# Performance work log

Measured on AMD Instinct MI355X. Metric: run time of the kernel, lower is better.

The kernel has to match this reference:

```python
import jax, jax.numpy as jnp
import numpy as np

BLANK = 0
NEG = jnp.float32(-1e30)  # finite stand-in for -inf (keeps logaddexp grads NaN-free)


def _ctc_loss(preds, targets, blank=BLANK):
    """CTC loss with fused log_softmax, zero_infinity, reduction='mean'.

    preds:   (N, T, C) raw logits
    targets: (N, L) int labels, 0 = padding/blank; target_lengths = count_nonzero
    """
    N, T, C = preds.shape
    L = targets.shape[1]
    S = 2 * L + 1  # extended label length (blanks interleaved)

    lp = jax.nn.log_softmax(preds, axis=-1)  # (N, T, C)

    # extended label sequence: blank, y1, blank, y2, ..., yL, blank
    ext = jnp.full((N, S), blank, dtype=targets.dtype).at[:, 1::2].set(targets)

    # gather log-probs of extended labels: (N, T, S) -> scan over T as (T, N, S)
    lp_ext = jax.vmap(lambda l, e: l[:, e])(lp, ext).transpose(1, 0, 2)

    # skip transition s-2 -> s allowed iff ext[s] != blank and ext[s] != ext[s-2]
    prev2 = jnp.pad(ext, ((0, 0), (2, 0)), constant_values=blank)[:, :S]
    skip_ok = (ext != blank) & (ext != prev2)  # (N, S)

    # alpha init at t=0
    alpha0 = jnp.full((N, S), NEG, dtype=lp.dtype)
    alpha0 = alpha0.at[:, 0].set(lp_ext[0, :, 0]).at[:, 1].set(lp_ext[0, :, 1])

    neg_col = jnp.full((N, 1), NEG, dtype=lp.dtype)

    def step(alpha, lp_t):
        a1 = jnp.concatenate([neg_col, alpha[:, :-1]], axis=1)
        a2 = jnp.concatenate([neg_col, neg_col, alpha[:, :-2]], axis=1)
        a2 = jnp.where(skip_ok, a2, NEG)
        alpha = jnp.logaddexp(jnp.logaddexp(alpha, a1), a2) + lp_t
        return alpha, None

    alpha, _ = jax.lax.scan(step, alpha0, lp_ext[1:])  # (N, S) at t = T-1

    tl = jnp.sum(targets != 0, axis=1)  # target lengths (pred lengths are all T)
    rows = jnp.arange(N)
    final = jnp.logaddexp(alpha[rows, 2 * tl], alpha[rows, 2 * tl - 1])

    # zero_infinity=True: zero out non-finite (vanished) losses
    loss = jnp.where(final < -1e29, 0.0, -final)
    # reduction='mean': divide each by its target length, then batch-mean
    return jnp.mean(loss / jnp.maximum(tl, 1).astype(loss.dtype))


def setup_inputs() -> dict:
    key = jax.random.key(0)
    k1, k2 = jax.random.split(key)
    preds = jax.random.normal(k1, (128, 1024, 256), dtype=jnp.float32)
    # labels in [1, C): nonzero so count_nonzero gives full target lengths
    targets = jax.random.randint(k2, (128, 128), 1, 256, dtype=jnp.int32)
    return {"preds": preds, "targets": targets}


def reference(preds, targets):
    return _ctc_loss(preds, targets)
```

## Files before the change

### kernel.cpp

```cpp
#include <hip/hip_runtime.h>

#define L2E 1.4426950408889634f
#define LN2D 0.6931471805599453

__device__ __forceinline__ void async_copy16(const float* g, float* l) {
    __builtin_amdgcn_global_load_lds(
        (const __attribute__((address_space(1))) void*)g,
        (__attribute__((address_space(3))) void*)l, 16, 0, 0);
}
__device__ __forceinline__ void wait_vm28() { __builtin_amdgcn_s_waitcnt(0x4F7C); }
__device__ __forceinline__ void wait_vm0()  { __builtin_amdgcn_s_waitcnt(0x0F70); }

__device__ __forceinline__ double dpp_sr1_f64(double x) {
    const int lo = __builtin_amdgcn_update_dpp(0, __double2loint(x), 0x138, 0xF, 0xF, true);
    const int hi = __builtin_amdgcn_update_dpp(0, __double2hiint(x), 0x138, 0xF, 0xF, true);
    return __hiloint2double(hi, lo);
}
__device__ __forceinline__ double dpp_sl1_f64(double x) {
    const int lo = __builtin_amdgcn_update_dpp(0, __double2loint(x), 0x130, 0xF, 0xF, true);
    const int hi = __builtin_amdgcn_update_dpp(0, __double2hiint(x), 0x130, 0xF, 0xF, true);
    return __hiloint2double(hi, lo);
}
__device__ __forceinline__ int wave_imax(int v) {
    int t;
#define DM(ctrl) t = __builtin_amdgcn_update_dpp(v, v, (ctrl), 0xF, 0xF, false); v = (v > t) ? v : t
    DM(0x111); DM(0x112); DM(0x114); DM(0x118);
    DM(0x142); DM(0x143);
#undef DM
    return __builtin_amdgcn_readlane(v, 63);
}

__global__ __launch_bounds__(256) void gather_kernel(const float* __restrict__ preds,
                                                     const int* __restrict__ targets,
                                                     float* __restrict__ gath,
                                                     float* __restrict__ blank) {
    constexpr int T = 1024, C = 256, L = 128;
    const int n = blockIdx.x >> 6;
    const int c = ((blockIdx.x & 63) << 2) + (threadIdx.x >> 6);
    const int lane = threadIdx.x & 63;
    const int w = threadIdx.x >> 6;

    const float* __restrict__ P = preds + ((size_t)n * T + (size_t)c * 4) * C;
    const int* __restrict__ tg = targets + (size_t)n * L;
    const int tgA = tg[2 * lane + 0];
    const int tgB = tg[2 * lane + 1];

    __shared__ float sRow[4][4][C];
    float m_k[4], r_k[4];
#pragma unroll
    for (int k = 0; k < 4; ++k) {
        const float4 v = reinterpret_cast<const float4*>(P + (size_t)k * C)[lane];
        reinterpret_cast<float4*>(&sRow[w][k][0])[lane] = v;
        float m = fmaxf(fmaxf(v.x, v.y), fmaxf(v.z, v.w));
#pragma unroll
        for (int off = 32; off; off >>= 1) m = fmaxf(m, __shfl_xor(m, off, 64));
        float s = exp2f((v.x - m) * L2E) + exp2f((v.y - m) * L2E) +
                  exp2f((v.z - m) * L2E) + exp2f((v.w - m) * L2E);
#pragma unroll
        for (int off = 32; off; off >>= 1) s += __shfl_xor(s, off, 64);
        m_k[k] = m; r_k[k] = 1.0f / s;
    }
    float4 gA, gB;
    gA.x = exp2f((sRow[w][0][tgA] - m_k[0]) * L2E) * r_k[0];
    gA.y = exp2f((sRow[w][1][tgA] - m_k[1]) * L2E) * r_k[1];
    gA.z = exp2f((sRow[w][2][tgA] - m_k[2]) * L2E) * r_k[2];
    gA.w = exp2f((sRow[w][3][tgA] - m_k[3]) * L2E) * r_k[3];
    gB.x = exp2f((sRow[w][0][tgB] - m_k[0]) * L2E) * r_k[0];
    gB.y = exp2f((sRow[w][1][tgB] - m_k[1]) * L2E) * r_k[1];
    gB.z = exp2f((sRow[w][2][tgB] - m_k[2]) * L2E) * r_k[2];
    gB.w = exp2f((sRow[w][3][tgB] - m_k[3]) * L2E) * r_k[3];

    float* gp = gath + ((size_t)n * 256 + c) * 512;
    *reinterpret_cast<float4*>(gp + 4 * lane) = gA;
    *reinterpret_cast<float4*>(gp + 256 + 4 * lane) = gB;
    if (lane == 0) {
        float4 b;
        b.x = exp2f((sRow[w][0][0] - m_k[0]) * L2E) * r_k[0];
        b.y = exp2f((sRow[w][1][0] - m_k[1]) * L2E) * r_k[1];
        b.z = exp2f((sRow[w][2][0] - m_k[2]) * L2E) * r_k[2];
        b.w = exp2f((sRow[w][3][0] - m_k[3]) * L2E) * r_k[3];
        *reinterpret_cast<float4*>(blank + (size_t)n * T + (size_t)c * 4) = b;
    }
}

__global__ __launch_bounds__(64) void ctc_alpha_kernel(const float* __restrict__ gath,
                                                       const float* __restrict__ blank,
                                                       const int* __restrict__ targets,
                                                       float* __restrict__ loss_out) {
    constexpr int T = 1024, L = 128;
    __shared__ float sG[16 * 512];
    __shared__ float sBlank[T];

    const int n = blockIdx.x;
    const int lane = threadIdx.x;
    const int* __restrict__ tg = targets + (size_t)n * L;

    const int tA = tg[2 * lane + 0];
    const int tB = tg[2 * lane + 1];
    int tPrev = __shfl_up(tB, 1, 64);
    if (lane == 0) tPrev = 0;
    const int skipAi = (tA != 0 && tA != tPrev) ? 1 : 0;
    const bool skipA = skipAi != 0;
    const bool skipB = (tB != 0) && (tB != tA);
    const double mBd = skipB ? 1.0 : 0.0;
    const double mA1d = (double)__shfl_down(skipAi, 1, 64);

    int cnt = (tA != 0) + (tB != 0);
#pragma unroll
    for (int off = 32; off; off >>= 1) cnt += __shfl_xor(cnt, off, 64);
    const int tl = cnt;
    int i1 = 2 * tl;       if (i1 > 256) i1 = 256;
    int i0 = 2 * tl - 1;   if (i0 < 0) i0 += 257;

    const float* __restrict__ gn = gath + (size_t)n * 131072;
    const float* __restrict__ bn = blank + (size_t)n * T;

    wait_vm0();

#pragma unroll
    for (int i = 0; i < 4; ++i) async_copy16(bn + i * 256 + lane * 4, &sBlank[i * 256]);
#pragma unroll
    for (int i = 0; i < 8; ++i) {
        async_copy16(gn + i * 512 + lane * 4,       &sG[i * 512]);
        async_copy16(gn + i * 512 + 256 + lane * 4, &sG[i * 512 + 256]);
        const int q = 255 - i;
        async_copy16(gn + q * 512 + lane * 4,       &sG[(8 + i) * 512]);
        async_copy16(gn + q * 512 + 256 + lane * 4, &sG[(8 + i) * 512 + 256]);
    }

    double A0, A1, A2, A3, A4;
    double B0, B1, B2, B3, B4;
    double scA = 1.0, scB = 1.0;
    int eA = 0, eB = 0, KA = 0, KB = 0;

    {
        const int s0 = 4 * lane;
        B0 = (s0 == i1 || s0 == i0) ? 1.0 : 0.0;
        B1 = (s0 + 1 == i1 || s0 + 1 == i0) ? 1.0 : 0.0;
        B2 = (s0 + 2 == i1 || s0 + 2 == i0) ? 1.0 : 0.0;
        B3 = (s0 + 3 == i1 || s0 + 3 == i0) ? 1.0 : 0.0;
        B4 = (lane == 63 && (i1 == 256 || i0 == 256)) ? 1.0 : 0.0;
    }

#define ASTEP(PB, PA, PB2) do {                                                 \
        const double p3 = dpp_sr1_f64(A3);                                      \
        const double u0 = A0 + p3;                                              \
        const double u1 = A1 + A0 + (skipA ? p3 : 0.0);                         \
        const double u2 = A2 + A1;                                              \
        const double u3 = A3 + A2 + (skipB ? A1 : 0.0);                         \
        const double u4 = A4 + A3;                                              \
        A0 = u0 * (PB); A1 = u1 * (PA); A2 = u2 * (PB);                         \
        A3 = u3 * (PB2); A4 = u4 * (PB);                                        \
    } while (0)

#define BSTEP(PBF, PAF, PBF2) do {                                              \
        const double pb_ = (PBF);                                               \
        const double g0 = pb_ * B0;                                             \
        const double g1 = (PAF) * B1;                                           \
        const double g2 = pb_ * B2;                                             \
        const double g3 = (PBF2) * B3;                                          \
        const double g4 = pb_ * B4;                                             \
        double G4 = dpp_sl1_f64(g0);                                            \
        G4 = (lane == 63) ? g4 : G4;                                            \
        const double G5 = dpp_sl1_f64(g1);                                      \
        B0 = g0 + g1;                                                           \
        B1 = fma(mBd, g3, g1 + g2);                                             \
        B2 = g2 + g3;                                                           \
        B3 = fma(mA1d, G5, g3 + G4);                                            \
        B4 = g4;                                                                \
    } while (0)

#define PAIRBODY(P_, FIRST_)  do {                                              \
        const int sl_ = (P_) & 7;                                               \
        wait_vm28();                                                            \
        const float4 aA = *reinterpret_cast<const float4*>(&sG[sl_ * 512 + 4 * lane]);        \
        const float4 aB = *reinterpret_cast<const float4*>(&sG[sl_ * 512 + 256 + 4 * lane]);  \
        const float4 ab = *reinterpret_cast<const float4*>(&sBlank[4 * (P_)]);                \
        const float4 bA = *reinterpret_cast<const float4*>(&sG[(8 + sl_) * 512 + 4 * lane]);       \
        const float4 bB = *reinterpret_cast<const float4*>(&sG[(8 + sl_) * 512 + 256 + 4 * lane]); \
        const float4 bb = *reinterpret_cast<const float4*>(&sBlank[4 * (255 - (P_))]);        \
        { const int cp = (P_) + 8, q = 247 - (P_);                              \
          async_copy16(gn + cp * 512 + lane * 4,       &sG[sl_ * 512]);         \
          async_copy16(gn + cp * 512 + 256 + lane * 4, &sG[sl_ * 512 + 256]);   \
          async_copy16(gn + q * 512 + lane * 4,        &sG[(8 + sl_) * 512]);   \
          async_copy16(gn + q * 512 + 256 + lane * 4,  &sG[(8 + sl_) * 512 + 256]); } \
        if (FIRST_) {                                                           \
            A0 = lane ? 0.0 : (double)ab.x;                                     \
            A1 = lane ? 0.0 : (double)aA.x;                                     \
            A2 = 0.0; A3 = 0.0; A4 = 0.0;                                       \
        } else {                                                                \
            ASTEP((double)ab.x, (double)aA.x, (double)aB.x);                    \
        }                                                                       \
        BSTEP((double)bb.w, (double)bA.w, (double)bB.w);                        \
        ASTEP((double)ab.y, (double)aA.y, (double)aB.y);                        \
        BSTEP((double)bb.z, (double)bA.z, (double)bB.z);                        \
        ASTEP((double)ab.z, (double)aA.z, (double)aB.z);                        \
        BSTEP((double)bb.y, (double)bA.y, (double)bB.y);                        \
        ASTEP((double)ab.w, (double)aA.w, (double)aB.w);                        \
        BSTEP((double)bb.x, (double)bA.x, (double)bB.x);                        \
    } while (0)

#define RESCALES() do {                                                         \
        A0 *= scA; A1 *= scA; A2 *= scA; A3 *= scA; A4 *= scA; KA += eA;        \
        B0 *= scB; B1 *= scB; B2 *= scB; B3 *= scB; B4 *= scB; KB += eB;        \
        const double ma = fmax(fmax(fmax(A0, A1), fmax(A2, A3)), A4);           \
        const double mb = fmax(fmax(fmax(B0, B1), fmax(B2, B3)), B4);           \
        int ea_ = ((__double2hiint(ma) >> 20) & 0x7FF) - 1023;                  \
        int eb_ = ((__double2hiint(mb) >> 20) & 0x7FF) - 1023;                  \
        ea_ = wave_imax(ea_); eb_ = wave_imax(eb_);                             \
        ea_ = ea_ < -960 ? -960 : (ea_ > 960 ? 960 : ea_);                      \
        eb_ = eb_ < -960 ? -960 : (eb_ > 960 ? 960 : eb_);                      \
        eA = ea_; scA = __hiloint2double((1023 - ea_) << 20, 0);                \
        eB = eb_; scB = __hiloint2double((1023 - eb_) << 20, 0);                \
    } while (0)

    PAIRBODY(0, true);
    for (int p = 1; p < 127; p += 2) {
        PAIRBODY(p, false);
        RESCALES();
        PAIRBODY(p + 1, false);
    }
    PAIRBODY(127, false);
    RESCALES();
    A0 *= scA; A1 *= scA; A2 *= scA; A3 *= scA; A4 *= scA; KA += eA;
    B0 *= scB; B1 *= scB; B2 *= scB; B3 *= scB; B4 *= scB; KB += eB;
#undef RESCALES
#undef PAIRBODY
#undef BSTEP
#undef ASTEP

    double S = A0 * B0 + A1 * B1 + A2 * B2 + A3 * B3;
    S += (lane == 63) ? A4 * B4 : 0.0;
#pragma unroll
    for (int off = 32; off; off >>= 1) S += __shfl_xor(S, off, 64);
    if (lane == 0) {
        const double loss = (S > 0.0) ? -(log2(S) + (double)(KA + KB)) * LN2D : 0.0;
        loss_out[n] = (float)(loss / (double)(tl > 0 ? tl : 1));
    }
}

__global__ __launch_bounds__(64) void reduce_kernel(const float* __restrict__ loss,
                                                    float* __restrict__ out, int N) {
    float s = 0.0f;
    for (int i = threadIdx.x; i < N; i += 64) s += loss[i];
#pragma unroll
    for (int off = 32; off; off >>= 1) s += __shfl_xor(s, off, 64);
    if (threadIdx.x == 0) out[0] = s / (float)N;
}

extern "C" void kernel_launch(void* const* d_in, const int* in_sizes, int n_in,
                              void* d_out, int out_size, void* d_ws, size_t ws_size,
                              hipStream_t stream) {
    const float* preds = (const float*)d_in[0];
    const int* targets = (const int*)d_in[1];
    const int N = in_sizes[1] / 128;
    const int T = 1024;

    float* gath = (float*)d_ws;
    float* blank = gath + (size_t)N * 131072;
    float* loss = blank + (size_t)N * T;
    float* out = (float*)d_out;

    gather_kernel<<<N * 64, 256, 0, stream>>>(preds, targets, gath, blank);
    ctc_alpha_kernel<<<N, 64, 0, stream>>>(gath, blank, targets, loss);
    reduce_kernel<<<1, 64, 0, stream>>>(loss, out, N);
}
```

Before: 267.6 us.

## Split forward and backward CTC recursions into separate wavefronts per block

The alpha kernel now runs with two wavefronts per sample: wave 0 runs the forward recursion and wave 1 the backward one, each with its own async LDS prefetch ring and rescaling. The two halves meet through shared memory after a barrier, and wave 0 forms the dot product and the loss. This removes the interleaving of two dependent chains on a single wave and lets the hardware schedule them on separate waves. In exchange it doubles the threads per block and adds a sync, plus shared-memory traffic for the exchange.

```diff
diff --git a/kernel.cpp b/kernel.cpp
--- a/kernel.cpp
+++ b/kernel.cpp
@@ -8,7 +8,7 @@
         (const __attribute__((address_space(1))) void*)g,
         (__attribute__((address_space(3))) void*)l, 16, 0, 0);
 }
-__device__ __forceinline__ void wait_vm28() { __builtin_amdgcn_s_waitcnt(0x4F7C); }
+__device__ __forceinline__ void wait_vm14() { __builtin_amdgcn_s_waitcnt(0x0F7E); }
 __device__ __forceinline__ void wait_vm0()  { __builtin_amdgcn_s_waitcnt(0x0F70); }
 
 __device__ __forceinline__ double dpp_sr1_f64(double x) {
@@ -83,16 +83,20 @@
     }
 }
 
-__global__ __launch_bounds__(64) void ctc_alpha_kernel(const float* __restrict__ gath,
-                                                       const float* __restrict__ blank,
-                                                       const int* __restrict__ targets,
-                                                       float* __restrict__ loss_out) {
+__global__ __launch_bounds__(128) void ctc_alpha_kernel(const float* __restrict__ gath,
+                                                        const float* __restrict__ blank,
+                                                        const int* __restrict__ targets,
+                                                        float* __restrict__ loss_out) {
     constexpr int T = 1024, L = 128;
     __shared__ float sG[16 * 512];
     __shared__ float sBlank[T];
+    __shared__ double xA[5][64];
+    __shared__ double xB[5][64];
+    __shared__ int xK[2];
 
     const int n = blockIdx.x;
-    const int lane = threadIdx.x;
+    const int w = threadIdx.x >> 6;
+    const int lane = threadIdx.x & 63;
     const int* __restrict__ tg = targets + (size_t)n * L;
 
     const int tA = tg[2 * lane + 0];
@@ -117,125 +121,151 @@
 
     wait_vm0();
 
-#pragma unroll
-    for (int i = 0; i < 4; ++i) async_copy16(bn + i * 256 + lane * 4, &sBlank[i * 256]);
-#pragma unroll
-    for (int i = 0; i < 8; ++i) {
-        async_copy16(gn + i * 512 + lane * 4,       &sG[i * 512]);
-        async_copy16(gn + i * 512 + 256 + lane * 4, &sG[i * 512 + 256]);
-        const int q = 255 - i;
-        async_copy16(gn + q * 512 + lane * 4,       &sG[(8 + i) * 512]);
-        async_copy16(gn + q * 512 + 256 + lane * 4, &sG[(8 + i) * 512 + 256]);
-    }
-
-    double A0, A1, A2, A3, A4;
-    double B0, B1, B2, B3, B4;
-    double scA = 1.0, scB = 1.0;
-    int eA = 0, eB = 0, KA = 0, KB = 0;
-
-    {
-        const int s0 = 4 * lane;
-        B0 = (s0 == i1 || s0 == i0) ? 1.0 : 0.0;
-        B1 = (s0 + 1 == i1 || s0 + 1 == i0) ? 1.0 : 0.0;
-        B2 = (s0 + 2 == i1 || s0 + 2 == i0) ? 1.0 : 0.0;
-        B3 = (s0 + 3 == i1 || s0 + 3 == i0) ? 1.0 : 0.0;
-        B4 = (lane == 63 && (i1 == 256 || i0 == 256)) ? 1.0 : 0.0;
-    }
+    double R0, R1, R2, R3, R4;
+    double sc = 1.0;
+    int e = 0, K = 0;
 
 #define ASTEP(PB, PA, PB2) do {                                                 \
-        const double p3 = dpp_sr1_f64(A3);                                      \
-        const double u0 = A0 + p3;                                              \
-        const double u1 = A1 + A0 + (skipA ? p3 : 0.0);                         \
-        const double u2 = A2 + A1;                                              \
-        const double u3 = A3 + A2 + (skipB ? A1 : 0.0);                         \
-        const double u4 = A4 + A3;                                              \
-        A0 = u0 * (PB); A1 = u1 * (PA); A2 = u2 * (PB);                         \
-        A3 = u3 * (PB2); A4 = u4 * (PB);                                        \
+        const double p3 = dpp_sr1_f64(R3);                                      \
+        const double u0 = R0 + p3;                                              \
+        const double u1 = R1 + R0 + (skipA ? p3 : 0.0);                         \
+        const double u2 = R2 + R1;                                              \
+        const double u3 = R3 + R2 + (skipB ? R1 : 0.0);                         \
+        const double u4 = R4 + R3;                                              \
+        R0 = u0 * (PB); R1 = u1 * (PA); R2 = u2 * (PB);                         \
+        R3 = u3 * (PB2); R4 = u4 * (PB);                                        \
     } while (0)
 
 #define BSTEP(PBF, PAF, PBF2) do {                                              \
         const double pb_ = (PBF);                                               \
-        const double g0 = pb_ * B0;                                             \
-        const double g1 = (PAF) * B1;                                           \
-        const double g2 = pb_ * B2;                                             \
-        const double g3 = (PBF2) * B3;                                          \
-        const double g4 = pb_ * B4;                                             \
+        const double g0 = pb_ * R0;                                             \
+        const double g1 = (PAF) * R1;                                           \
+        const double g2 = pb_ * R2;                                             \
+        const double g3 = (PBF2) * R3;                                          \
+        const double g4 = pb_ * R4;                                             \
         double G4 = dpp_sl1_f64(g0);                                            \
         G4 = (lane == 63) ? g4 : G4;                                            \
         const double G5 = dpp_sl1_f64(g1);                                      \
-        B0 = g0 + g1;                                                           \
-        B1 = fma(mBd, g3, g1 + g2);                                             \
-        B2 = g2 + g3;                                                           \
-        B3 = fma(mA1d, G5, g3 + G4);                                            \
-        B4 = g4;                                                                \
-    } while (0)
-
-#define PAIRBODY(P_, FIRST_)  do {                                              \
+        R0 = g0 + g1;                                                           \
+        R1 = fma(mBd, g3, g1 + g2);                                             \
+        R2 = g2 + g3;                                                           \
+        R3 = fma(mA1d, G5, g3 + G4);                                            \
+        R4 = g4;                                                                \
+    } while (0)
+
+#define RESC() do {                                                             \
+        R0 *= sc; R1 *= sc; R2 *= sc; R3 *= sc; R4 *= sc; K += e;               \
+        const double m_ = fmax(fmax(fmax(R0, R1), fmax(R2, R3)), R4);           \
+        int e_ = ((__double2hiint(m_) >> 20) & 0x7FF) - 1023;                   \
+        e_ = wave_imax(e_);                                                     \
+        e_ = e_ < -960 ? -960 : (e_ > 960 ? 960 : e_);                          \
+        e = e_; sc = __hiloint2double((1023 - e_) << 20, 0);                    \
+    } while (0)
+
+#define APAIR(P_, FIRST_) do {                                                  \
         const int sl_ = (P_) & 7;                                               \
-        wait_vm28();                                                            \
+        wait_vm14();                                                            \
         const float4 aA = *reinterpret_cast<const float4*>(&sG[sl_ * 512 + 4 * lane]);        \
         const float4 aB = *reinterpret_cast<const float4*>(&sG[sl_ * 512 + 256 + 4 * lane]);  \
         const float4 ab = *reinterpret_cast<const float4*>(&sBlank[4 * (P_)]);                \
-        const float4 bA = *reinterpret_cast<const float4*>(&sG[(8 + sl_) * 512 + 4 * lane]);       \
-        const float4 bB = *reinterpret_cast<const float4*>(&sG[(8 + sl_) * 512 + 256 + 4 * lane]); \
-        const float4 bb = *reinterpret_cast<const float4*>(&sBlank[4 * (255 - (P_))]);        \
-        { const int cp = (P_) + 8, q = 247 - (P_);                              \
+        { const int cp = (P_) + 8;                                              \
           async_copy16(gn + cp * 512 + lane * 4,       &sG[sl_ * 512]);         \
-          async_copy16(gn + cp * 512 + 256 + lane * 4, &sG[sl_ * 512 + 256]);   \
-          async_copy16(gn + q * 512 + lane * 4,        &sG[(8 + sl_) * 512]);   \
-          async_copy16(gn + q * 512 + 256 + lane * 4,  &sG[(8 + sl_) * 512 + 256]); } \
+          async_copy16(gn + cp * 512 + 256 + lane * 4, &sG[sl_ * 512 + 256]); } \
         if (FIRST_) {                                                           \
-            A0 = lane ? 0.0 : (double)ab.x;                                     \
-            A1 = lane ? 0.0 : (double)aA.x;                                     \
-            A2 = 0.0; A3 = 0.0; A4 = 0.0;                                       \
+            R0 = lane ? 0.0 : (double)ab.x;                                     \
+            R1 = lane ? 0.0 : (double)aA.x;                                     \
+            R2 = 0.0; R3 = 0.0; R4 = 0.0;                                       \
         } else {                                                                \
             ASTEP((double)ab.x, (double)aA.x, (double)aB.x);                    \
         }                                                                       \
+        ASTEP((double)ab.y, (double)aA.y, (double)aB.y);                        \
+        ASTEP((double)ab.z, (double)aA.z, (double)aB.z);                        \
+        ASTEP((double)ab.w, (double)aA.w, (double)aB.w);                        \
+    } while (0)
+
+#define BPAIR(P_) do {                                                          \
+        const int sl_ = 8 + ((P_) & 7);                                         \
+        wait_vm14();                                                            \
+        const float4 bA = *reinterpret_cast<const float4*>(&sG[sl_ * 512 + 4 * lane]);        \
+        const float4 bB = *reinterpret_cast<const float4*>(&sG[sl_ * 512 + 256 + 4 * lane]);  \
+        const float4 bb = *reinterpret_cast<const float4*>(&sBlank[4 * (255 - (P_))]);        \
+        { const int q = 247 - (P_);                                             \
+          async_copy16(gn + q * 512 + lane * 4,       &sG[sl_ * 512]);          \
+          async_copy16(gn + q * 512 + 256 + lane * 4, &sG[sl_ * 512 + 256]); }  \
         BSTEP((double)bb.w, (double)bA.w, (double)bB.w);                        \
-        ASTEP((double)ab.y, (double)aA.y, (double)aB.y);                        \
         BSTEP((double)bb.z, (double)bA.z, (double)bB.z);                        \
-        ASTEP((double)ab.z, (double)aA.z, (double)aB.z);                        \
         BSTEP((double)bb.y, (double)bA.y, (double)bB.y);                        \
-        ASTEP((double)ab.w, (double)aA.w, (double)aB.w);                        \
         BSTEP((double)bb.x, (double)bA.x, (double)bB.x);                        \
     } while (0)
 
-#define RESCALES() do {                                                         \
-        A0 *= scA; A1 *= scA; A2 *= scA; A3 *= scA; A4 *= scA; KA += eA;        \
-        B0 *= scB; B1 *= scB; B2 *= scB; B3 *= scB; B4 *= scB; KB += eB;        \
-        const double ma = fmax(fmax(fmax(A0, A1), fmax(A2, A3)), A4);           \
-        const double mb = fmax(fmax(fmax(B0, B1), fmax(B2, B3)), B4);           \
-        int ea_ = ((__double2hiint(ma) >> 20) & 0x7FF) - 1023;                  \
-        int eb_ = ((__double2hiint(mb) >> 20) & 0x7FF) - 1023;                  \
-        ea_ = wave_imax(ea_); eb_ = wave_imax(eb_);                             \
-        ea_ = ea_ < -960 ? -960 : (ea_ > 960 ? 960 : ea_);                      \
-        eb_ = eb_ < -960 ? -960 : (eb_ > 960 ? 960 : eb_);                      \
-        eA = ea_; scA = __hiloint2double((1023 - ea_) << 20, 0);                \
-        eB = eb_; scB = __hiloint2double((1023 - eb_) << 20, 0);                \
-    } while (0)
-
-    PAIRBODY(0, true);
-    for (int p = 1; p < 127; p += 2) {
-        PAIRBODY(p, false);
-        RESCALES();
-        PAIRBODY(p + 1, false);
-    }
-    PAIRBODY(127, false);
-    RESCALES();
-    A0 *= scA; A1 *= scA; A2 *= scA; A3 *= scA; A4 *= scA; KA += eA;
-    B0 *= scB; B1 *= scB; B2 *= scB; B3 *= scB; B4 *= scB; KB += eB;
-#undef RESCALES
-#undef PAIRBODY
+    if (w == 0) {
+        async_copy16(bn + lane * 4,       &sBlank[0]);
+        async_copy16(bn + 256 + lane * 4, &sBlank[256]);
+#pragma unroll
+        for (int i = 0; i < 8; ++i) {
+            async_copy16(gn + i * 512 + lane * 4,       &sG[i * 512]);
+            async_copy16(gn + i * 512 + 256 + lane * 4, &sG[i * 512 + 256]);
+        }
+        APAIR(0, true);
+        for (int p = 1; p < 127; p += 2) {
+            APAIR(p, false);
+            RESC();
+            APAIR(p + 1, false);
+        }
+        APAIR(127, false);
+        RESC();
+        R0 *= sc; R1 *= sc; R2 *= sc; R3 *= sc; R4 *= sc; K += e;
+        xA[0][lane] = R0; xA[1][lane] = R1; xA[2][lane] = R2;
+        xA[3][lane] = R3; xA[4][lane] = R4;
+        if (lane == 0) xK[0] = K;
+    } else {
+        async_copy16(bn + 512 + lane * 4, &sBlank[512]);
+        async_copy16(bn + 768 + lane * 4, &sBlank[768]);
+#pragma unroll
+        for (int i = 0; i < 8; ++i) {
+            const int q = 255 - i;
+            async_copy16(gn + q * 512 + lane * 4,       &sG[(8 + i) * 512]);
+            async_copy16(gn + q * 512 + 256 + lane * 4, &sG[(8 + i) * 512 + 256]);
+        }
+        {
+            const int s0 = 4 * lane;
+            R0 = (s0 == i1 || s0 == i0) ? 1.0 : 0.0;
+            R1 = (s0 + 1 == i1 || s0 + 1 == i0) ? 1.0 : 0.0;
+            R2 = (s0 + 2 == i1 || s0 + 2 == i0) ? 1.0 : 0.0;
+            R3 = (s0 + 3 == i1 || s0 + 3 == i0) ? 1.0 : 0.0;
+            R4 = (lane == 63 && (i1 == 256 || i0 == 256)) ? 1.0 : 0.0;
+        }
+        BPAIR(0);
+        for (int p = 1; p < 127; p += 2) {
+            BPAIR(p);
+            RESC();
+            BPAIR(p + 1);
+        }
+        BPAIR(127);
+        RESC();
+        R0 *= sc; R1 *= sc; R2 *= sc; R3 *= sc; R4 *= sc; K += e;
+        xB[0][lane] = R0; xB[1][lane] = R1; xB[2][lane] = R2;
+        xB[3][lane] = R3; xB[4][lane] = R4;
+        if (lane == 0) xK[1] = K;
+    }
+#undef BPAIR
+#undef APAIR
+#undef RESC
 #undef BSTEP
 #undef ASTEP
 
-    double S = A0 * B0 + A1 * B1 + A2 * B2 + A3 * B3;
-    S += (lane == 63) ? A4 * B4 : 0.0;
-#pragma unroll
-    for (int off = 32; off; off >>= 1) S += __shfl_xor(S, off, 64);
-    if (lane == 0) {
-        const double loss = (S > 0.0) ? -(log2(S) + (double)(KA + KB)) * LN2D : 0.0;
-        loss_out[n] = (float)(loss / (double)(tl > 0 ? tl : 1));
+    __syncthreads();
+
+    if (w == 0) {
+        double S = R0 * xB[0][lane] + R1 * xB[1][lane] + R2 * xB[2][lane] + R3 * xB[3][lane];
+        S += (lane == 63) ? R4 * xB[4][lane] : 0.0;
+#pragma unroll
+        for (int off = 32; off; off >>= 1) S += __shfl_xor(S, off, 64);
+        if (lane == 0) {
+            const int Ktot = K + xK[1];
+            const double loss = (S > 0.0) ? -(log2(S) + (double)Ktot) * LN2D : 0.0;
+            loss_out[n] = (float)(loss / (double)(tl > 0 ? tl : 1));
+        }
     }
 }
 
@@ -262,6 +292,6 @@
     float* out = (float*)d_out;
 
     gather_kernel<<<N * 64, 256, 0, stream>>>(preds, targets, gath, blank);
-    ctc_alpha_kernel<<<N, 64, 0, stream>>>(gath, blank, targets, loss);
+    ctc_alpha_kernel<<<N, 128, 0, stream>>>(gath, blank, targets, loss);
     reduce_kernel<<<1, 64, 0, stream>>>(loss, out, N);
 }
```

Result: faster. 243.1 us (-9.1%).
